# Optimization experiments

Hardware: AMD Instinct MI355X
Metric: run time of the kernel (lower is better)

## Reference

```python
import jax, jax.numpy as jnp
import numpy as np

B, D, N, H = 1024, 512, 16, 512  # batch, latent, branches, hidden


def _lrelu(v):
    return jnp.where(v >= 0, v, 0.1 * v)  # LeakyReLU(0.1)


def setup_inputs() -> dict:
    key = jax.random.key(0)
    ks = jax.random.split(key, 9)
    s = 0.02
    return {
        "x": jax.random.normal(ks[0], (B, D, N), dtype=jnp.float32),
        "Ws1": jax.random.normal(ks[1], (D, D), dtype=jnp.float32) * s,
        "bs1": jnp.zeros((D,), dtype=jnp.float32),
        "Ws2": jax.random.normal(ks[2], (D, D), dtype=jnp.float32) * s,
        "bs2": jnp.zeros((D,), dtype=jnp.float32),
        # per-branch binary classifiers: Linear(D,H)+LeakyReLU+Linear(H,1)
        "Wc1": jax.random.normal(ks[3], (N, D, H), dtype=jnp.float32) * s,
        "bc1": jnp.zeros((N, H), dtype=jnp.float32),
        "Wc2": jax.random.normal(ks[4], (N, H), dtype=jnp.float32) * s,
        "bc2": jnp.zeros((N,), dtype=jnp.float32),
    }


def reference(x, Ws1, bs1, Ws2, bs2, Wc1, bc1, Wc2, bc2):
    # x: [B, D, N] -> per-branch tokens [B, N, D]
    xb = jnp.transpose(x, (0, 2, 1))
    # shared MLP applied to every branch slice (same weights)
    h = _lrelu(xb @ Ws1 + bs1)
    shared = _lrelu(h @ Ws2 + bs2)  # [B, N, D]
    # per-branch classifier on its own branch slice -> sigmoid probs
    h1 = _lrelu(jnp.einsum('bnd,ndh->bnh', shared, Wc1) + bc1)
    logits = jnp.einsum('bnh,nh->bn', h1, Wc2) + bc2  # [B, N]
    out = jax.nn.sigmoid(logits)[:, None, :]  # [B, 1, N]
    # full pass: concat branch slices along batch (branch-major), every
    # classifier applied to the full stack -> raw logits
    full_in = jnp.transpose(shared, (1, 0, 2)).reshape(N * B, D)  # [M, D]
    h2 = _lrelu(jnp.einsum('md,ndh->mnh', full_in, Wc1) + bc1)  # [M, N, H]
    full_logits = jnp.einsum('mnh,nh->mn', h2, Wc2) + bc2  # [M, N]
    full_out = full_logits[:, None, :]  # [N*B, 1, N]
    return (out, full_out)
```

## Files before the change

kernel.cpp:

```cpp
#include <hip/hip_runtime.h>
#include <hip/hip_bf16.h>
#include <stdint.h>

#define Bq 1024
#define Dq 512
#define Nq 16
#define Hq 512
#define Mq (Bq*Nq)

typedef short v8s  __attribute__((ext_vector_type(8)));
typedef float v16f __attribute__((ext_vector_type(16)));

typedef __attribute__((address_space(3))) unsigned int as3_u32;
typedef __attribute__((address_space(1))) const unsigned int as1_u32;

__device__ __forceinline__ unsigned short f2bf(float f) {
  union { float f; unsigned u; } v; v.f = f;
  return (unsigned short)((v.u + 0x7fffu + ((v.u >> 16) & 1u)) >> 16);
}

__global__ void k_transpose_x(const float* __restrict__ x, unsigned short* __restrict__ xb) {
  __shared__ float lds[Dq][Nq + 1];
  const int b = blockIdx.x;
  const float* xi = x + (size_t)b * Dq * Nq;
  const int t = threadIdx.x;
  for (int p = 0; p < (Dq*Nq)/256; ++p) {
    int i = t + p*256;
    lds[i >> 4][i & (Nq-1)] = xi[i];
  }
  __syncthreads();
  unsigned short* o = xb + (size_t)b * Nq * Dq;
  for (int p = 0; p < (Dq*Nq)/256; ++p) {
    int i = t + p*256;
    o[i] = f2bf(lds[i & (Dq-1)][i >> 9]);
  }
}

__global__ void k_transpose_w(const float* __restrict__ Ws1, const float* __restrict__ Ws2,
                              const float* __restrict__ Wc1,
                              unsigned short* __restrict__ Ws1t, unsigned short* __restrict__ Ws2t,
                              unsigned short* __restrict__ Wc1t) {
  __shared__ float tile[32][33];
  const int z = blockIdx.z;
  const float* in;
  unsigned short* out;
  if (z == 0)      { in = Ws1; out = Ws1t; }
  else if (z == 1) { in = Ws2; out = Ws2t; }
  else             { in = Wc1 + (size_t)(z-2) * 512 * 512; out = Wc1t + (size_t)(z-2) * 512 * 512; }
  const int tx = threadIdx.x, ty = threadIdx.y;
  const int c0 = blockIdx.x * 32, r0 = blockIdx.y * 32;
#pragma unroll
  for (int j = 0; j < 4; ++j)
    tile[ty + j*8][tx] = in[(size_t)(r0 + ty + j*8) * 512 + c0 + tx];
  __syncthreads();
#pragma unroll
  for (int j = 0; j < 4; ++j) {
    int c = c0 + ty + j*8;
    int r = r0 + tx;
    out[(size_t)c * 512 + r] = f2bf(tile[tx][ty + j*8]);
  }
}

template<int MODE>
__global__ __launch_bounds__(256, 2)
void k_gemm(const unsigned short* __restrict__ A,
            const unsigned short* __restrict__ Bt,
            const float* __restrict__ bias,
            void* __restrict__ out_,
            const float* __restrict__ w2,
            int permute) {
  constexpr int BM = 128, BN = 128, BK = 128, KD = 512, NKT = KD / BK;
  __shared__ __align__(16) unsigned short As[BM][BK];
  __shared__ __align__(16) unsigned short Bs[BN][BK];

  const int t = threadIdx.x;
  const int wave = t >> 6, lane = t & 63;
  const int wrm = wave >> 1, wrn = wave & 1;
  const int l32 = lane & 31, kh0 = lane >> 5;
  const int bm = blockIdx.x * BM, bn = blockIdx.y * BN;
  const int z = blockIdx.z;

  const unsigned short* Bz = Bt + (size_t)z * KD * 512;
  const float* biasz = bias + (size_t)z * 512;

  const int srow = lane >> 4;
  const int sslot = lane & 15;

  auto stage = [&](int kt) {
#pragma unroll
    for (int j = 0; j < 16; ++j) {
      const int g = wave * 16 + j;
      const bool isA = (g < 32);
      const int r0 = (isA ? g : g - 32) * 4;
      const int row = r0 + srow;
      const int cg = sslot ^ ((row >> 1) & 7);
      const unsigned short* gp = isA ? &A [(size_t)(bm + row) * KD + kt*BK + cg*8]
                                     : &Bz[(size_t)(bn + row) * KD + kt*BK + cg*8];
      as3_u32* d = isA ? (as3_u32*)&As[r0][0] : (as3_u32*)&Bs[r0][0];
      __builtin_amdgcn_global_load_lds((as1_u32*)gp, d, 16, 0, 0);
    }
  };

  v16f acc[2][2] = {};

  stage(0);

  for (int kt = 0; kt < NKT; ++kt) {
    __syncthreads();
    const int ra0 = wrm*64 + l32, rb0 = wrn*64 + l32;
#pragma unroll
    for (int ks = 0; ks < 8; ++ks) {
      v8s af[2], bf[2];
#pragma unroll
      for (int mi = 0; mi < 2; ++mi) {
        int ra = ra0 + mi*32;
        af[mi] = *(const v8s*)&As[ra][(((ks*2 + kh0) ^ ((ra >> 1) & 7))) * 8];
      }
#pragma unroll
      for (int ni = 0; ni < 2; ++ni) {
        int rb = rb0 + ni*32;
        bf[ni] = *(const v8s*)&Bs[rb][(((ks*2 + kh0) ^ ((rb >> 1) & 7))) * 8];
      }
#pragma unroll
      for (int mi = 0; mi < 2; ++mi)
#pragma unroll
        for (int ni = 0; ni < 2; ++ni)
          acc[mi][ni] = __builtin_amdgcn_mfma_f32_32x32x16_bf16(af[mi], bf[ni], acc[mi][ni], 0, 0, 0);
    }
    __syncthreads();
    if (kt + 1 < NKT) stage(kt + 1);
  }

  if (MODE == 0) {
    unsigned short* O = (unsigned short*)out_;
#pragma unroll
    for (int mi = 0; mi < 2; ++mi) {
#pragma unroll
      for (int ni = 0; ni < 2; ++ni) {
        int col = bn + wrn*64 + ni*32 + l32;
        float bcol = biasz[col];
#pragma unroll
        for (int reg = 0; reg < 16; ++reg) {
          int rl = (reg & 3) + 8*(reg >> 2) + 4*kh0;
          int grow = bm + wrm*64 + mi*32 + rl;
          int orow = permute ? ((grow & 15) * Bq + (grow >> 4)) : grow;
          float v = acc[mi][ni][reg] + bcol;
          v = v >= 0.f ? v : 0.1f * v;
          O[(size_t)orow * 512 + col] = f2bf(v);
        }
      }
    }
  } else {
    float* FL = (float*)out_;
    const float* w2z = w2 + (size_t)z * 512;
#pragma unroll
    for (int mi = 0; mi < 2; ++mi) {
#pragma unroll
      for (int reg = 0; reg < 16; ++reg) {
        int rl = (reg & 3) + 8*(reg >> 2) + 4*kh0;
        float s = 0.f;
#pragma unroll
        for (int ni = 0; ni < 2; ++ni) {
          int col = bn + wrn*64 + ni*32 + l32;
          float v = acc[mi][ni][reg] + biasz[col];
          v = v >= 0.f ? v : 0.1f * v;
          s += v * w2z[col];
        }
#pragma unroll
        for (int off = 1; off < 32; off <<= 1)
          s += __shfl_xor(s, off, 64);
        if (l32 == 0) {
          int grow = bm + wrm*64 + mi*32 + rl;
          atomicAdd(&FL[(size_t)grow * Nq + z], s);
        }
      }
    }
  }
}

__global__ void k_final(const float* __restrict__ fl, const float* __restrict__ bc2,
                        float* __restrict__ out) {
  int i = blockIdx.x * 256 + threadIdx.x;
  int m = i >> 4, n = i & 15;
  float v = fl[i] + bc2[n];
  out[Mq + i] = v;
  if (n == (m >> 10)) {
    int b = m & (Bq - 1);
    out[b * Nq + n] = 1.f / (1.f + __expf(-v));
  }
}

extern "C" void kernel_launch(void* const* d_in, const int* in_sizes, int n_in,
                              void* d_out, int out_size, void* d_ws, size_t ws_size,
                              hipStream_t stream) {
  (void)in_sizes; (void)n_in; (void)out_size; (void)ws_size;
  const float* x   = (const float*)d_in[0];
  const float* Ws1 = (const float*)d_in[1];
  const float* bs1 = (const float*)d_in[2];
  const float* Ws2 = (const float*)d_in[3];
  const float* bs2 = (const float*)d_in[4];
  const float* Wc1 = (const float*)d_in[5];
  const float* bc1 = (const float*)d_in[6];
  const float* Wc2 = (const float*)d_in[7];
  const float* bc2 = (const float*)d_in[8];

  char* ws = (char*)d_ws;
  unsigned short* Xb   = (unsigned short*)(ws);
  unsigned short* Hbuf = (unsigned short*)(ws + (size_t)16*1024*1024);
  unsigned short* Sm   = (unsigned short*)(ws + (size_t)32*1024*1024);
  unsigned short* Ws1t = (unsigned short*)(ws + (size_t)48*1024*1024);
  unsigned short* Ws2t = (unsigned short*)(ws + (size_t)48*1024*1024 + 512*1024);
  unsigned short* Wc1t = (unsigned short*)(ws + (size_t)49*1024*1024);
  float*          FL   = (float*)         (ws + (size_t)57*1024*1024);

  hipMemsetAsync(FL, 0, (size_t)Mq * Nq * sizeof(float), stream);

  k_transpose_x<<<Bq, 256, 0, stream>>>(x, Xb);
  k_transpose_w<<<dim3(16,16,18), dim3(32,8), 0, stream>>>(Ws1, Ws2, Wc1, Ws1t, Ws2t, Wc1t);

  k_gemm<0><<<dim3(128,4,1), 256, 0, stream>>>(Xb,   Ws1t, bs1, Hbuf, nullptr, 0);
  k_gemm<0><<<dim3(128,4,1), 256, 0, stream>>>(Hbuf, Ws2t, bs2, Sm,   nullptr, 1);
  k_gemm<1><<<dim3(128,4,16), 256, 0, stream>>>(Sm, Wc1t, bc1, FL, Wc2, 0);

  k_final<<<(Mq*Nq)/256, 256, 0, stream>>>(FL, bc2, (float*)d_out);
}
```

Baseline: 385.3 us.

## Warp-specialize GEMM with producer waves and double-buffered smaller K tiles

The GEMM kernel now launches 512 threads: four producer waves issue global-to-LDS loads into a double-buffered shared-memory tile, while four consumer waves run the MFMA loop on the other buffer. BK shrinks from 128 to 32 so two buffers fit, and the XOR swizzle is adapted to 4 slots. The aim is to overlap memory loads with compute, which the old stage-then-compute loop serialized. In exchange there are more barriers per K (16 iterations instead of 4), and the smaller K tile may reduce MFMA work per sync.

```diff
diff --git a/kernel.cpp b/kernel.cpp
--- a/kernel.cpp
+++ b/kernel.cpp
@@ -62,64 +62,71 @@
 }
 
 template<int MODE>
-__global__ __launch_bounds__(256, 2)
+__global__ __launch_bounds__(512, 4)
 void k_gemm(const unsigned short* __restrict__ A,
             const unsigned short* __restrict__ Bt,
             const float* __restrict__ bias,
             void* __restrict__ out_,
             const float* __restrict__ w2,
             int permute) {
-  constexpr int BM = 128, BN = 128, BK = 128, KD = 512, NKT = KD / BK;
-  __shared__ __align__(16) unsigned short As[BM][BK];
-  __shared__ __align__(16) unsigned short Bs[BN][BK];
+  constexpr int BM = 128, BN = 128, BK = 32, KD = 512, NKT = KD / BK;
+  __shared__ __align__(16) unsigned short As[2][BM][BK];
+  __shared__ __align__(16) unsigned short Bs[2][BN][BK];
 
   const int t = threadIdx.x;
   const int wave = t >> 6, lane = t & 63;
+  const int bm = blockIdx.x * BM, bn = blockIdx.y * BN;
+  const int z = blockIdx.z;
+  const unsigned short* Bz = Bt + (size_t)z * KD * 512;
+  const float* biasz = bias + (size_t)z * 512;
+
+  if (wave >= 4) {
+    const int pw = wave - 4;
+    const int lrow = lane >> 2, lslot = lane & 3;
+    auto stage = [&](int buf, int kt) {
+#pragma unroll
+      for (int i = pw; i < 16; i += 4) {
+        const bool isA = (i < 8);
+        const int r0 = (isA ? i : i - 8) * 16;
+        const int row = r0 + lrow;
+        const int cg = lslot ^ ((row >> 1) & 3);
+        const unsigned short* g = isA ? &A [(size_t)(bm + row) * KD + kt*BK + cg*8]
+                                      : &Bz[(size_t)(bn + row) * KD + kt*BK + cg*8];
+        as3_u32* d = isA ? (as3_u32*)&As[buf][r0][0] : (as3_u32*)&Bs[buf][r0][0];
+        __builtin_amdgcn_global_load_lds((as1_u32*)g, d, 16, 0, 0);
+      }
+    };
+    stage(0, 0);
+    asm volatile("s_waitcnt vmcnt(0)" ::: "memory");
+    __syncthreads();
+    for (int kt = 0; kt < NKT; ++kt) {
+      if (kt + 1 < NKT) stage((kt + 1) & 1, kt + 1);
+      asm volatile("s_waitcnt vmcnt(0)" ::: "memory");
+      __syncthreads();
+    }
+    return;
+  }
+
   const int wrm = wave >> 1, wrn = wave & 1;
   const int l32 = lane & 31, kh0 = lane >> 5;
-  const int bm = blockIdx.x * BM, bn = blockIdx.y * BN;
-  const int z = blockIdx.z;
-
-  const unsigned short* Bz = Bt + (size_t)z * KD * 512;
-  const float* biasz = bias + (size_t)z * 512;
-
-  const int srow = lane >> 4;
-  const int sslot = lane & 15;
-
-  auto stage = [&](int kt) {
-#pragma unroll
-    for (int j = 0; j < 16; ++j) {
-      const int g = wave * 16 + j;
-      const bool isA = (g < 32);
-      const int r0 = (isA ? g : g - 32) * 4;
-      const int row = r0 + srow;
-      const int cg = sslot ^ ((row >> 1) & 7);
-      const unsigned short* gp = isA ? &A [(size_t)(bm + row) * KD + kt*BK + cg*8]
-                                     : &Bz[(size_t)(bn + row) * KD + kt*BK + cg*8];
-      as3_u32* d = isA ? (as3_u32*)&As[r0][0] : (as3_u32*)&Bs[r0][0];
-      __builtin_amdgcn_global_load_lds((as1_u32*)gp, d, 16, 0, 0);
-    }
-  };
-
   v16f acc[2][2] = {};
 
-  stage(0);
-
+  __syncthreads();
   for (int kt = 0; kt < NKT; ++kt) {
-    __syncthreads();
-    const int ra0 = wrm*64 + l32, rb0 = wrn*64 + l32;
-#pragma unroll
-    for (int ks = 0; ks < 8; ++ks) {
+    const int cur = kt & 1;
+#pragma unroll
+    for (int kh = 0; kh < 2; ++kh) {
+      const int c = kh*2 + kh0;
       v8s af[2], bf[2];
 #pragma unroll
       for (int mi = 0; mi < 2; ++mi) {
-        int ra = ra0 + mi*32;
-        af[mi] = *(const v8s*)&As[ra][(((ks*2 + kh0) ^ ((ra >> 1) & 7))) * 8];
+        int ra = wrm*64 + mi*32 + l32;
+        af[mi] = *(const v8s*)&As[cur][ra][(c ^ ((ra >> 1) & 3)) * 8];
       }
 #pragma unroll
       for (int ni = 0; ni < 2; ++ni) {
-        int rb = rb0 + ni*32;
-        bf[ni] = *(const v8s*)&Bs[rb][(((ks*2 + kh0) ^ ((rb >> 1) & 7))) * 8];
+        int rb = wrn*64 + ni*32 + l32;
+        bf[ni] = *(const v8s*)&Bs[cur][rb][(c ^ ((rb >> 1) & 3)) * 8];
       }
 #pragma unroll
       for (int mi = 0; mi < 2; ++mi)
@@ -128,7 +135,6 @@
           acc[mi][ni] = __builtin_amdgcn_mfma_f32_32x32x16_bf16(af[mi], bf[ni], acc[mi][ni], 0, 0, 0);
     }
     __syncthreads();
-    if (kt + 1 < NKT) stage(kt + 1);
   }
 
   if (MODE == 0) {
@@ -218,9 +224,9 @@
   k_transpose_x<<<Bq, 256, 0, stream>>>(x, Xb);
   k_transpose_w<<<dim3(16,16,18), dim3(32,8), 0, stream>>>(Ws1, Ws2, Wc1, Ws1t, Ws2t, Wc1t);
 
-  k_gemm<0><<<dim3(128,4,1), 256, 0, stream>>>(Xb,   Ws1t, bs1, Hbuf, nullptr, 0);
-  k_gemm<0><<<dim3(128,4,1), 256, 0, stream>>>(Hbuf, Ws2t, bs2, Sm,   nullptr, 1);
-  k_gemm<1><<<dim3(128,4,16), 256, 0, stream>>>(Sm, Wc1t, bc1, FL, Wc2, 0);
+  k_gemm<0><<<dim3(128,4,1), 512, 0, stream>>>(Xb,   Ws1t, bs1, Hbuf, nullptr, 0);
+  k_gemm<0><<<dim3(128,4,1), 512, 0, stream>>>(Hbuf, Ws2t, bs2, Sm,   nullptr, 1);
+  k_gemm<1><<<dim3(128,4,16), 512, 0, stream>>>(Sm, Wc1t, bc1, FL, Wc2, 0);
 
   k_final<<<(Mq*Nq)/256, 256, 0, stream>>>(FL, bc2, (float*)d_out);
 }
```

After: 413.3 us. 7.3% more time.
